# Kernel optimization log

Hardware: AMD Instinct MI355X
Metric: run time of the kernel (lower is better)

Reference implementation:

```python
import jax, jax.numpy as jnp
import numpy as np

B, N, F, H = 2, 2048, 1024, 16
HD = F // H
SQRT_D = float(np.sqrt(F))  # note: module scales by sqrt(in_c), not sqrt(head_dim)


def setup_inputs() -> dict:
    key = jax.random.key(0)
    ks = jax.random.split(key, 9)
    s = 1.0 / np.sqrt(F)
    mk = lambda k: jax.random.uniform(k, (F, F), jnp.float32, -s, s)
    mb = lambda k: jax.random.uniform(k, (F,), jnp.float32, -s, s)
    return {
        "x": jax.random.normal(ks[0], (B, N, F), jnp.float32),
        "Wq": mk(ks[1]), "bq": mb(ks[2]),
        "Wk": mk(ks[3]), "bk": mb(ks[4]),
        "Wv": mk(ks[5]), "bv": mb(ks[6]),
        "Wo": mk(ks[7]), "bo": mb(ks[8]),
    }


def reference(x, Wq, bq, Wk, bk, Wv, bv, Wo, bo):
    b, n, f = x.shape
    # projections (torch Linear: x @ W.T + b); view to (b, n, h, hd)
    q = (x @ Wq.T + bq).reshape(b, n, H, HD)
    k = (x @ Wk.T + bk).reshape(b, n, H, HD)
    v = (x @ Wv.T + bv).reshape(b, n, H, HD)
    score = jnp.einsum('bihd,bjhd->bhij', q, k)
    attn = jax.nn.softmax(score / SQRT_D, axis=-1)
    o = jnp.einsum('bhij,bjhd->bihd', attn, v).reshape(b, n, f)
    return o @ Wo.T + bo
```

## Files before the change

kernel.cpp:

```cpp
#include <hip/hip_runtime.h>
#include <hip/hip_bf16.h>
#include <stdint.h>
#include <stddef.h>

typedef __bf16 bf16;
typedef __attribute__((ext_vector_type(8))) __bf16 bf16x8;
typedef __attribute__((ext_vector_type(4))) __bf16 bf16x4;
typedef __attribute__((ext_vector_type(2))) __bf16 bf16x2;
typedef __attribute__((ext_vector_type(4))) float f32x4;

#define MFMA16(a, b, c) __builtin_amdgcn_mfma_f32_16x16x32_bf16(a, b, c, 0, 0, 0)

#define BB 2
#define SEQ 2048
#define FDIM 1024
#define NH 16
#define HD 64
#define M_TOK 4096
#define N_QKV 3072

#define CSC 0.04508422f

__device__ __forceinline__ void gll16(const bf16* g, bf16* l) {
    __builtin_amdgcn_global_load_lds(
        (const __attribute__((address_space(1))) void*)g,
        (__attribute__((address_space(3))) void*)l, 16, 0, 0);
}

__device__ __forceinline__ bf16 pack_bf16(float f) {
    uint32_t u = __builtin_bit_cast(uint32_t, f);
    uint16_t h = (uint16_t)((u + 0x8000u) >> 16);
    return __builtin_bit_cast(bf16, h);
}

__device__ __forceinline__ uint32_t pk2(float a, float b) {
#if __has_builtin(__builtin_amdgcn_cvt_pk_bf16_f32)
    bf16x2 t = __builtin_amdgcn_cvt_pk_bf16_f32(a, b);
    return __builtin_bit_cast(uint32_t, t);
#else
    uint32_t ua = __builtin_bit_cast(uint32_t, a) + 0x8000u;
    uint32_t ub = __builtin_bit_cast(uint32_t, b) + 0x8000u;
    return __builtin_amdgcn_perm(ub, ua, 0x07060302);
#endif
}

__global__ __launch_bounds__(256) void convert_k(
    const float* __restrict__ x,
    const float* __restrict__ Wq, const float* __restrict__ bq,
    const float* __restrict__ Wk, const float* __restrict__ bk,
    const float* __restrict__ Wv, const float* __restrict__ bv,
    const float* __restrict__ Wo,
    bf16* __restrict__ xb, bf16* __restrict__ Wcat, bf16* __restrict__ Wob,
    float* __restrict__ bcat)
{
    const int tid = blockIdx.x * blockDim.x + threadIdx.x;
    const int nt = gridDim.x * blockDim.x;
    const int NX4 = M_TOK * FDIM / 4;
    const int NW4 = FDIM * FDIM / 4;

    for (int i = tid; i < NX4; i += nt) {
        float4 v = ((const float4*)x)[i];
        bf16x4 o; o[0] = (bf16)v.x; o[1] = (bf16)v.y; o[2] = (bf16)v.z; o[3] = (bf16)v.w;
        ((bf16x4*)xb)[i] = o;
    }
    for (int i = tid; i < NW4; i += nt) {
        float4 v = ((const float4*)Wq)[i];
        bf16x4 o;
        o[0] = (bf16)(v.x * CSC); o[1] = (bf16)(v.y * CSC);
        o[2] = (bf16)(v.z * CSC); o[3] = (bf16)(v.w * CSC);
        ((bf16x4*)Wcat)[i] = o;
        v = ((const float4*)Wk)[i];
        o[0] = (bf16)v.x; o[1] = (bf16)v.y; o[2] = (bf16)v.z; o[3] = (bf16)v.w;
        ((bf16x4*)Wcat)[NW4 + i] = o;
        v = ((const float4*)Wv)[i];
        o[0] = (bf16)v.x; o[1] = (bf16)v.y; o[2] = (bf16)v.z; o[3] = (bf16)v.w;
        ((bf16x4*)Wcat)[2 * NW4 + i] = o;
        v = ((const float4*)Wo)[i];
        o[0] = (bf16)v.x; o[1] = (bf16)v.y; o[2] = (bf16)v.z; o[3] = (bf16)v.w;
        ((bf16x4*)Wob)[i] = o;
    }
    for (int i = tid; i < FDIM; i += nt) {
        bcat[i] = bq[i] * CSC;
        bcat[FDIM + i] = bk[i];
        bcat[2 * FDIM + i] = bv[i];
    }
}

template<int MT>
__global__ __launch_bounds__(256) void gemm_bt(
    const bf16* __restrict__ A,
    const bf16* __restrict__ Bw,
    const float* __restrict__ bias,
    bf16* __restrict__ Cb,
    float* __restrict__ Cf,
    bf16* __restrict__ VtOut,
    int M, int N, int K)
{
    constexpr int RI = MT / 32;
    __shared__ __align__(16) bf16 As[2][MT * 32];
    __shared__ __align__(16) bf16 Bs[2][128 * 32];

    const int tid = threadIdx.x;
    const int lane = tid & 63;
    const int wave = tid >> 6;
    const int m0 = blockIdx.y * MT;
    const int n0 = blockIdx.x * 128;
    const int wm = (wave >> 1) * (MT / 2);
    const int wn = (wave & 1) * 64;
    const int lrow = lane & 15;
    const int lk8 = (lane >> 4) * 8;

    f32x4 acc[RI][4] = {};

    const int srow = wave * 16 + (lane >> 2);
    const int scol = (lane & 3) * 8;
    const bf16* Ag = A + (size_t)(m0 + srow) * K + scol;
    const bf16* Bg = Bw + (size_t)(n0 + srow) * K + scol;
    const int wo = (wave * 16) * 32;

    gll16(Ag, &As[0][wo]);
    if (MT == 128) gll16(Ag + (size_t)64 * K, &As[0][wo + 2048]);
    gll16(Bg, &Bs[0][wo]);
    gll16(Bg + (size_t)64 * K, &Bs[0][wo + 2048]);

    for (int k0 = 0, it = 0; k0 < K; k0 += 32, ++it) {
        const int cur = it & 1;
        __syncthreads();

        if (k0 + 32 < K) {
            const int nxt = cur ^ 1;
            gll16(Ag + k0 + 32, &As[nxt][wo]);
            if (MT == 128) gll16(Ag + (size_t)64 * K + k0 + 32, &As[nxt][wo + 2048]);
            gll16(Bg + k0 + 32, &Bs[nxt][wo]);
            gll16(Bg + (size_t)64 * K + k0 + 32, &Bs[nxt][wo + 2048]);
        }

        bf16x8 af[RI], bfr[4];
#pragma unroll
        for (int s = 0; s < RI; ++s)
            af[s] = *(const bf16x8*)&As[cur][(wm + s * 16 + lrow) * 32 + lk8];
#pragma unroll
        for (int s = 0; s < 4; ++s)
            bfr[s] = *(const bf16x8*)&Bs[cur][(wn + s * 16 + lrow) * 32 + lk8];
#pragma unroll
        for (int i = 0; i < RI; ++i)
#pragma unroll
            for (int j = 0; j < 4; ++j)
                acc[i][j] = MFMA16(af[i], bfr[j], acc[i][j]);
    }

    const int r0 = (lane >> 4) * 4;
    if (MT == 128 && VtOut && n0 >= 2048) {
        const int bql = (m0 >> 11);
#pragma unroll
        for (int i = 0; i < RI; ++i) {
#pragma unroll
            for (int j = 0; j < 4; ++j) {
                const int col = n0 + wn + j * 16 + lrow;
                const float bsv = bias[col];
                const int vh = col - 2048;
                const int row = m0 + wm + i * 16 + r0;
                const int jj = row & (SEQ - 1);
                const int g = jj & 63;
                const int jj2 = (jj & ~63) | ((g >> 5) << 5)
                              | (((g >> 2) & 3) << 3) | (((g >> 4) & 1) << 2);
                bf16x4 vv;
#pragma unroll
                for (int r = 0; r < 4; ++r)
                    vv[r] = pack_bf16(acc[i][j][r] + bsv);
                *(bf16x4*)&VtOut[((size_t)bql * 16 * 64 + vh) * SEQ + jj2] = vv;
            }
        }
        return;
    }
#pragma unroll
    for (int i = 0; i < RI; ++i) {
#pragma unroll
        for (int j = 0; j < 4; ++j) {
            const int col = n0 + wn + j * 16 + lrow;
            const float bsv = bias[col];
#pragma unroll
            for (int r = 0; r < 4; ++r) {
                const int row = m0 + wm + i * 16 + r0 + r;
                const float v = acc[i][j][r] + bsv;
                if (Cb) Cb[(size_t)row * N + col] = pack_bf16(v);
                else    Cf[(size_t)row * N + col] = v;
            }
        }
    }
}

__global__ __launch_bounds__(256) void attn_k(
    const bf16* __restrict__ QKV,
    const bf16* __restrict__ Vt,
    bf16* __restrict__ O)
{
    const int bx = blockIdx.x;
    const int bh = (bx & 7) + 8 * ((bx >> 3) & 3);
    const int qblk = bx >> 5;
    const int b = bh >> 4;
    const int h = bh & 15;
    const int lane = threadIdx.x & 63;
    const int wave = threadIdx.x >> 6;
    const int lrow = lane & 15;
    const int quad = lane >> 4;
    const int lk8 = quad * 8;

    __shared__ __align__(16) bf16 Ks[2][2][128 * 32];
    __shared__ __align__(16) bf16 Vs[2][4][64 * 32];

    const size_t base = (size_t)b * SEQ * N_QKV;
    const bf16* Qp = QKV + base + h * HD;
    const bf16* Kp = QKV + base + FDIM + h * HD;
    const bf16* Vtp = Vt + (size_t)bh * HD * SEQ;

    const int qr0 = qblk * 128 + wave * 32;

    bf16x8 qf[2][2];
#pragma unroll
    for (int qt = 0; qt < 2; ++qt)
#pragma unroll
        for (int ks = 0; ks < 2; ++ks)
            qf[qt][ks] = *(const bf16x8*)(Qp + (size_t)(qr0 + qt * 16 + lrow) * N_QKV
                                          + ks * 32 + lk8);

    bf16x8 ones8;
#pragma unroll
    for (int e = 0; e < 8; ++e) ones8[e] = (bf16)1.0f;

    const f32x4 zf = {0.f, 0.f, 0.f, 0.f};

    f32x4 o[2][4] = {};
    f32x4 o4[2] = {};

    const int srow = wave * 16 + (lane >> 2);
    const int scol = (lane & 3) * 8;
    const bf16* kg = Kp + (size_t)srow * N_QKV + scol;
    const bf16* vg = Vtp + (size_t)srow * SEQ + scol;
    const int wo = (wave * 16) * 32;

    gll16(kg, &Ks[0][0][wo]);
    gll16(kg + 32, &Ks[0][1][wo]);
    gll16(kg + (size_t)64 * N_QKV, &Ks[0][0][wo + 2048]);
    gll16(kg + (size_t)64 * N_QKV + 32, &Ks[0][1][wo + 2048]);
    gll16(vg, &Vs[0][0][wo]);
    gll16(vg + 32, &Vs[0][1][wo]);
    gll16(vg + 64, &Vs[0][2][wo]);
    gll16(vg + 96, &Vs[0][3][wo]);
    kg += (size_t)128 * N_QKV;
    vg += 128;

    for (int jt = 0; jt < SEQ / 128; ++jt) {
        const int cur = jt & 1;
        __syncthreads();

        if (jt + 1 < SEQ / 128) {
            const int nxt = cur ^ 1;
            gll16(kg, &Ks[nxt][0][wo]);
            gll16(kg + 32, &Ks[nxt][1][wo]);
            gll16(kg + (size_t)64 * N_QKV, &Ks[nxt][0][wo + 2048]);
            gll16(kg + (size_t)64 * N_QKV + 32, &Ks[nxt][1][wo + 2048]);
            gll16(vg, &Vs[nxt][0][wo]);
            gll16(vg + 32, &Vs[nxt][1][wo]);
            gll16(vg + 64, &Vs[nxt][2][wo]);
            gll16(vg + 96, &Vs[nxt][3][wo]);
            kg += (size_t)128 * N_QKV;
            vg += 128;
        }

#pragma unroll
        for (int p = 0; p < 4; ++p) {
            f32x4 Sp[2][2];
#pragma unroll
            for (int m = 0; m < 2; ++m) {
                const int jn = 2 * p + m;
                bf16x8 kb0 = *(const bf16x8*)&Ks[cur][0][(jn * 16 + lrow) * 32 + lk8];
                bf16x8 kb1 = *(const bf16x8*)&Ks[cur][1][(jn * 16 + lrow) * 32 + lk8];
                Sp[m][0] = MFMA16(kb0, qf[0][0], zf);
                Sp[m][0] = MFMA16(kb1, qf[0][1], Sp[m][0]);
                Sp[m][1] = MFMA16(kb0, qf[1][0], zf);
                Sp[m][1] = MFMA16(kb1, qf[1][1], Sp[m][1]);
            }

            union { bf16x8 v; uint32_t d[4]; } pb[2];
#pragma unroll
            for (int qt = 0; qt < 2; ++qt) {
                const f32x4 s0 = Sp[0][qt];
                const f32x4 s1 = Sp[1][qt];
                pb[qt].d[0] = pk2(__builtin_amdgcn_exp2f(s0[0]),
                                  __builtin_amdgcn_exp2f(s0[1]));
                pb[qt].d[1] = pk2(__builtin_amdgcn_exp2f(s0[2]),
                                  __builtin_amdgcn_exp2f(s0[3]));
                pb[qt].d[2] = pk2(__builtin_amdgcn_exp2f(s1[0]),
                                  __builtin_amdgcn_exp2f(s1[1]));
                pb[qt].d[3] = pk2(__builtin_amdgcn_exp2f(s1[2]),
                                  __builtin_amdgcn_exp2f(s1[3]));
            }

            o4[0] = MFMA16(ones8, pb[0].v, o4[0]);
            o4[1] = MFMA16(ones8, pb[1].v, o4[1]);
#pragma unroll
            for (int df = 0; df < 4; ++df) {
                bf16x8 vA = *(const bf16x8*)&Vs[cur][p][(df * 16 + lrow) * 32 + lk8];
                o[0][df] = MFMA16(vA, pb[0].v, o[0][df]);
                o[1][df] = MFMA16(vA, pb[1].v, o[1][df]);
            }
        }
    }

#pragma unroll
    for (int qt = 0; qt < 2; ++qt) {
        const float inv = 1.0f / o4[qt][0];
        const int q = qr0 + qt * 16 + lrow;
#pragma unroll
        for (int df = 0; df < 4; ++df) {
            bf16x4 vv;
#pragma unroll
            for (int r = 0; r < 4; ++r)
                vv[r] = pack_bf16(o[qt][df][r] * inv);
            *(bf16x4*)&O[(size_t)(b * SEQ + q) * FDIM + h * HD + df * 16 + quad * 4] = vv;
        }
    }
}

extern "C" void kernel_launch(void* const* d_in, const int* in_sizes, int n_in,
                              void* d_out, int out_size, void* d_ws, size_t ws_size,
                              hipStream_t stream) {
    (void)in_sizes; (void)n_in; (void)out_size; (void)ws_size;
    const float* x  = (const float*)d_in[0];
    const float* Wq = (const float*)d_in[1];
    const float* bq = (const float*)d_in[2];
    const float* Wk = (const float*)d_in[3];
    const float* bk = (const float*)d_in[4];
    const float* Wv = (const float*)d_in[5];
    const float* bv = (const float*)d_in[6];
    const float* Wo = (const float*)d_in[7];
    const float* bo = (const float*)d_in[8];
    float* out = (float*)d_out;

    char* ws = (char*)d_ws;
    bf16* xb    = (bf16*)(ws);
    bf16* Wcat  = (bf16*)(ws + 8388608);
    bf16* Wob   = (bf16*)(ws + 14680064);
    float* bcat = (float*)(ws + 16777216);
    bf16* QKV   = (bf16*)(ws + 16789504);
    bf16* Vt    = (bf16*)(ws + 41955328);
    bf16* Ob    = xb;

    convert_k<<<dim3(1024), dim3(256), 0, stream>>>(x, Wq, bq, Wk, bk, Wv, bv, Wo,
                                                    xb, Wcat, Wob, bcat);
    gemm_bt<128><<<dim3(N_QKV / 128, M_TOK / 128), dim3(256), 0, stream>>>(
        xb, Wcat, bcat, QKV, nullptr, Vt, M_TOK, N_QKV, FDIM);
    attn_k<<<dim3((SEQ / 128) * BB * NH), dim3(256), 0, stream>>>(QKV, Vt, Ob);
    gemm_bt<64><<<dim3(FDIM / 128, M_TOK / 64), dim3(256), 0, stream>>>(
        Ob, Wob, bo, nullptr, out, nullptr, M_TOK, FDIM, FDIM);
}
```

Baseline: 191.0 us.

## Give each attention wave 64 query rows with 2 waves per block and split K/V loading

The attention kernel now runs 2 waves per block instead of 4, and each wave handles 64 query rows (4 MFMA tiles) instead of 32. Each K and V fragment read from LDS is therefore reused across twice as many query tiles, which halves LDS read traffic per unit of MFMA work. The tile loads are split so wave 0 loads K and wave 1 loads V. The cost is more accumulator and Q registers per wave, possibly lower occupancy, and fewer waves per CU available to hide latency.

```diff
diff --git a/kernel.cpp b/kernel.cpp
--- a/kernel.cpp
+++ b/kernel.cpp
@@ -190,7 +190,7 @@
     }
 }
 
-__global__ __launch_bounds__(256) void attn_k(
+__global__ __launch_bounds__(128) void attn_k(
     const bf16* __restrict__ QKV,
     const bf16* __restrict__ Vt,
     bf16* __restrict__ O)
@@ -214,11 +214,11 @@
     const bf16* Kp = QKV + base + FDIM + h * HD;
     const bf16* Vtp = Vt + (size_t)bh * HD * SEQ;
 
-    const int qr0 = qblk * 128 + wave * 32;
-
-    bf16x8 qf[2][2];
-#pragma unroll
-    for (int qt = 0; qt < 2; ++qt)
+    const int qr0 = qblk * 128 + wave * 64;
+
+    bf16x8 qf[4][2];
+#pragma unroll
+    for (int qt = 0; qt < 4; ++qt)
 #pragma unroll
         for (int ks = 0; ks < 2; ++ks)
             qf[qt][ks] = *(const bf16x8*)(Qp + (size_t)(qr0 + qt * 16 + lrow) * N_QKV
@@ -230,23 +230,27 @@
 
     const f32x4 zf = {0.f, 0.f, 0.f, 0.f};
 
-    f32x4 o[2][4] = {};
-    f32x4 o4[2] = {};
-
-    const int srow = wave * 16 + (lane >> 2);
-    const int scol = (lane & 3) * 8;
-    const bf16* kg = Kp + (size_t)srow * N_QKV + scol;
-    const bf16* vg = Vtp + (size_t)srow * SEQ + scol;
-    const int wo = (wave * 16) * 32;
-
-    gll16(kg, &Ks[0][0][wo]);
-    gll16(kg + 32, &Ks[0][1][wo]);
-    gll16(kg + (size_t)64 * N_QKV, &Ks[0][0][wo + 2048]);
-    gll16(kg + (size_t)64 * N_QKV + 32, &Ks[0][1][wo + 2048]);
-    gll16(vg, &Vs[0][0][wo]);
-    gll16(vg + 32, &Vs[0][1][wo]);
-    gll16(vg + 64, &Vs[0][2][wo]);
-    gll16(vg + 96, &Vs[0][3][wo]);
+    f32x4 o[4][4] = {};
+    f32x4 o4[4] = {};
+
+    const int sr = lane >> 2;
+    const int sc = (lane & 3) * 8;
+    const bf16* kg = Kp + (size_t)sr * N_QKV + sc;
+    const bf16* vg = Vtp + (size_t)sr * SEQ + sc;
+
+    if (wave == 0) {
+#pragma unroll
+        for (int i = 0; i < 8; ++i) {
+            gll16(kg + (size_t)i * 16 * N_QKV, &Ks[0][0][i * 16 * 32]);
+            gll16(kg + (size_t)i * 16 * N_QKV + 32, &Ks[0][1][i * 16 * 32]);
+        }
+    } else {
+#pragma unroll
+        for (int p = 0; p < 4; ++p)
+#pragma unroll
+            for (int i = 0; i < 4; ++i)
+                gll16(vg + (size_t)i * 16 * SEQ + p * 32, &Vs[0][p][i * 16 * 32]);
+    }
     kg += (size_t)128 * N_QKV;
     vg += 128;
 
@@ -256,35 +260,41 @@
 
         if (jt + 1 < SEQ / 128) {
             const int nxt = cur ^ 1;
-            gll16(kg, &Ks[nxt][0][wo]);
-            gll16(kg + 32, &Ks[nxt][1][wo]);
-            gll16(kg + (size_t)64 * N_QKV, &Ks[nxt][0][wo + 2048]);
-            gll16(kg + (size_t)64 * N_QKV + 32, &Ks[nxt][1][wo + 2048]);
-            gll16(vg, &Vs[nxt][0][wo]);
-            gll16(vg + 32, &Vs[nxt][1][wo]);
-            gll16(vg + 64, &Vs[nxt][2][wo]);
-            gll16(vg + 96, &Vs[nxt][3][wo]);
+            if (wave == 0) {
+#pragma unroll
+                for (int i = 0; i < 8; ++i) {
+                    gll16(kg + (size_t)i * 16 * N_QKV, &Ks[nxt][0][i * 16 * 32]);
+                    gll16(kg + (size_t)i * 16 * N_QKV + 32, &Ks[nxt][1][i * 16 * 32]);
+                }
+            } else {
+#pragma unroll
+                for (int p = 0; p < 4; ++p)
+#pragma unroll
+                    for (int i = 0; i < 4; ++i)
+                        gll16(vg + (size_t)i * 16 * SEQ + p * 32, &Vs[nxt][p][i * 16 * 32]);
+            }
             kg += (size_t)128 * N_QKV;
             vg += 128;
         }
 
 #pragma unroll
         for (int p = 0; p < 4; ++p) {
-            f32x4 Sp[2][2];
+            f32x4 Sp[2][4];
 #pragma unroll
             for (int m = 0; m < 2; ++m) {
                 const int jn = 2 * p + m;
                 bf16x8 kb0 = *(const bf16x8*)&Ks[cur][0][(jn * 16 + lrow) * 32 + lk8];
                 bf16x8 kb1 = *(const bf16x8*)&Ks[cur][1][(jn * 16 + lrow) * 32 + lk8];
-                Sp[m][0] = MFMA16(kb0, qf[0][0], zf);
-                Sp[m][0] = MFMA16(kb1, qf[0][1], Sp[m][0]);
-                Sp[m][1] = MFMA16(kb0, qf[1][0], zf);
-                Sp[m][1] = MFMA16(kb1, qf[1][1], Sp[m][1]);
-            }
-
-            union { bf16x8 v; uint32_t d[4]; } pb[2];
-#pragma unroll
-            for (int qt = 0; qt < 2; ++qt) {
+#pragma unroll
+                for (int qt = 0; qt < 4; ++qt) {
+                    Sp[m][qt] = MFMA16(kb0, qf[qt][0], zf);
+                    Sp[m][qt] = MFMA16(kb1, qf[qt][1], Sp[m][qt]);
+                }
+            }
+
+            union { bf16x8 v; uint32_t d[4]; } pb[4];
+#pragma unroll
+            for (int qt = 0; qt < 4; ++qt) {
                 const f32x4 s0 = Sp[0][qt];
                 const f32x4 s1 = Sp[1][qt];
                 pb[qt].d[0] = pk2(__builtin_amdgcn_exp2f(s0[0]),
@@ -295,21 +305,21 @@
                                   __builtin_amdgcn_exp2f(s1[1]));
                 pb[qt].d[3] = pk2(__builtin_amdgcn_exp2f(s1[2]),
                                   __builtin_amdgcn_exp2f(s1[3]));
-            }
-
-            o4[0] = MFMA16(ones8, pb[0].v, o4[0]);
-            o4[1] = MFMA16(ones8, pb[1].v, o4[1]);
+                o4[qt] = MFMA16(ones8, pb[qt].v, o4[qt]);
+            }
+
 #pragma unroll
             for (int df = 0; df < 4; ++df) {
                 bf16x8 vA = *(const bf16x8*)&Vs[cur][p][(df * 16 + lrow) * 32 + lk8];
-                o[0][df] = MFMA16(vA, pb[0].v, o[0][df]);
-                o[1][df] = MFMA16(vA, pb[1].v, o[1][df]);
-            }
-        }
-    }
-
-#pragma unroll
-    for (int qt = 0; qt < 2; ++qt) {
+#pragma unroll
+                for (int qt = 0; qt < 4; ++qt)
+                    o[qt][df] = MFMA16(vA, pb[qt].v, o[qt][df]);
+            }
+        }
+    }
+
+#pragma unroll
+    for (int qt = 0; qt < 4; ++qt) {
         const float inv = 1.0f / o4[qt][0];
         const int q = qr0 + qt * 16 + lrow;
 #pragma unroll
@@ -351,7 +361,7 @@
                                                     xb, Wcat, Wob, bcat);
     gemm_bt<128><<<dim3(N_QKV / 128, M_TOK / 128), dim3(256), 0, stream>>>(
         xb, Wcat, bcat, QKV, nullptr, Vt, M_TOK, N_QKV, FDIM);
-    attn_k<<<dim3((SEQ / 128) * BB * NH), dim3(256), 0, stream>>>(QKV, Vt, Ob);
+    attn_k<<<dim3((SEQ / 128) * BB * NH), dim3(128), 0, stream>>>(QKV, Vt, Ob);
     gemm_bt<64><<<dim3(FDIM / 128, M_TOK / 64), dim3(256), 0, stream>>>(
         Ob, Wob, bo, nullptr, out, nullptr, M_TOK, FDIM, FDIM);
 }
```

After: 192.7 us. No clear change (+0.9%).
